# Performance work log

Hardware: AMD Instinct MI355X
Metric: run time of the kernel (lower is better)

Reference implementation:

```python
import jax, jax.numpy as jnp
import numpy as np

# dims
B = 16        # batch
S = 32        # question seq len
H = 768       # bert-base hidden
E = 200000    # num entities
T = 200000    # padded triples per example
R = 500       # num relations
STEPS = 3     # num_steps
WAYS = 2      # num_ways


def setup_inputs() -> dict:
    key = jax.random.key(0)
    ks = jax.random.split(key, 10)
    # one-hot head entity per example (start distribution)
    head_ids = jax.random.randint(ks[0], (B,), 0, E)
    heads = jnp.zeros((B, E), jnp.float32).at[jnp.arange(B), head_ids].set(1.0)
    q_embeddings = jax.random.normal(ks[1], (B, H), jnp.float32)
    q_word_h = jax.random.normal(ks[2], (B, S, H), jnp.float32)
    attention_mask = jnp.ones((B, S), jnp.float32)
    # padded per-example triples (sub, rel, obj)
    sub = jax.random.randint(ks[3], (B, T), 0, E)
    rel = jax.random.randint(ks[4], (B, T), 0, R)
    obj = jax.random.randint(ks[5], (B, T), 0, E)
    triples = jnp.stack([sub, rel, obj], axis=-1).astype(jnp.int32)  # [B,T,3]
    scale = 0.02
    step_W = jax.random.normal(ks[6], (WAYS, STEPS, H, H), jnp.float32) * scale
    step_b = jnp.zeros((WAYS, STEPS, H), jnp.float32)
    rel_W = jax.random.normal(ks[7], (WAYS, H, R), jnp.float32) * scale
    rel_b = jnp.zeros((WAYS, R), jnp.float32)
    hop_W = jax.random.normal(ks[8], (WAYS, H, STEPS), jnp.float32) * scale
    hop_b = jnp.zeros((WAYS, STEPS), jnp.float32)
    return dict(heads=heads, q_embeddings=q_embeddings, q_word_h=q_word_h,
                attention_mask=attention_mask, step_W=step_W, step_b=step_b,
                rel_W=rel_W, rel_b=rel_b, hop_W=hop_W, hop_b=hop_b,
                triples=triples)


def _propagate(last_e, triples, rel_dist):
    # last_e: [E], triples: [T,3], rel_dist: [R] -> [E]
    sub, rel, obj = triples[:, 0], triples[:, 1], triples[:, 2]
    obj_p = last_e[sub] * rel_dist[rel]                 # gather + gate  [T]
    return jax.ops.segment_sum(obj_p, obj, num_segments=E)  # scatter-add [E]


def reference(heads, q_embeddings, q_word_h, attention_mask,
              step_W, step_b, rel_W, rel_b, hop_W, hop_b, triples):
    e_score = []
    for w in range(WAYS):
        last_e = heads                                   # [B,E]
        ent_probs = []
        for t in range(STEPS):
            cq_t = jnp.tanh(q_embeddings @ step_W[w, t] + step_b[w, t])   # [B,H]
            q_logits = jnp.einsum('bh,bsh->bs', cq_t, q_word_h)            # [B,S]
            q_dist = jax.nn.softmax(q_logits, axis=1) * attention_mask
            q_dist = q_dist / (jnp.sum(q_dist, axis=1, keepdims=True) + 1e-6)
            ctx_h = jnp.einsum('bs,bsh->bh', q_dist, q_word_h)             # [B,H]
            rel_dist = jax.nn.sigmoid(ctx_h @ rel_W[w] + rel_b[w])         # [B,R]
            last_e = jax.vmap(_propagate)(last_e, triples, rel_dist)      # [B,E]
            # renormalize entries > 1 (detached divisor, as in original)
            z = jax.lax.stop_gradient(jnp.where(last_e > 1.0, last_e, 1.0))
            last_e = last_e / z
            ent_probs.append(last_e)
        hop_res = jnp.stack(ent_probs, axis=1)                             # [B,STEPS,E]
        hop_attn = jax.nn.softmax(q_embeddings @ hop_W[w] + hop_b[w], axis=1)  # [B,STEPS]
        e_score.append(jnp.einsum('bse,bs->be', hop_res, hop_attn))
    return jnp.prod(jnp.stack(e_score), axis=0)                            # [B,E]
```

## Files before the change

kernel.cpp:

```cpp
#include <hip/hip_runtime.h>
#include <math.h>

#define NB 16
#define NS 32
#define NH 768
#define NE 200000
#define NT 200000
#define NR 500
#define NSTEPS 3
#define NWAYS 2

#define HSZ 2048
#define AHSZ 4096
#define BMW 6272

typedef unsigned int u32;

__device__ __forceinline__ int fhash(int e) { return (int)(((u32)e * 2654435761u) >> 21); }
__device__ __forceinline__ int ahash(int e) { return (int)(((u32)e * 2654435761u) >> 20); }

__global__ __launch_bounds__(256) void dense_kernel(
    const float* __restrict__ qe, const float* __restrict__ qwh,
    const float* __restrict__ mask,
    const float* __restrict__ stepW, const float* __restrict__ stepB,
    const float* __restrict__ relW, const float* __restrict__ relB,
    const float* __restrict__ hopW, const float* __restrict__ hopB,
    float* __restrict__ rel, float* __restrict__ hop)
{
    int blk = blockIdx.x;
    int b = blk % NB;
    int wt = blk / NB;
    int w = wt / NSTEPS;
    int t = wt % NSTEPS;

    __shared__ float s_qe[NH];
    __shared__ float s_part[4][NH];
    __shared__ float s_cq[NH];
    __shared__ float s_ctx[NH];
    __shared__ float s_sm[NS];

    int tid = threadIdx.x;
    int lane = tid & 63, wv = tid >> 6;

    for (int h = tid; h < NH; h += 256) s_qe[h] = qe[b * NH + h];
    __syncthreads();

    {
        const float* W = stepW + (size_t)wt * NH * NH;
        float acc[12];
#pragma unroll
        for (int q = 0; q < 12; ++q) acc[q] = 0.f;
        int h0 = wv * 192;
#pragma unroll 2
        for (int hh = 0; hh < 192; ++hh) {
            int h = h0 + hh;
            float qv = s_qe[h];
            const float* row = W + (size_t)h * NH + lane;
#pragma unroll
            for (int q = 0; q < 12; ++q) acc[q] += qv * row[q * 64];
        }
#pragma unroll
        for (int q = 0; q < 12; ++q) s_part[wv][lane + q * 64] = acc[q];
    }
    __syncthreads();
    for (int j = tid; j < NH; j += 256) {
        float a = s_part[0][j] + s_part[1][j] + s_part[2][j] + s_part[3][j] + stepB[wt * NH + j];
        s_cq[j] = tanhf(a);
    }
    __syncthreads();

    {
        int s = tid >> 3, l = tid & 7;
        const float* row = qwh + ((size_t)b * NS + s) * NH;
        float a = 0.f;
        for (int h = l; h < NH; h += 8) a += s_cq[h] * row[h];
        a += __shfl_down(a, 4, 8);
        a += __shfl_down(a, 2, 8);
        a += __shfl_down(a, 1, 8);
        if (l == 0) s_sm[s] = a;
    }
    __syncthreads();
    if (tid == 0) {
        float mx = -1e30f;
        for (int s = 0; s < NS; ++s) mx = fmaxf(mx, s_sm[s]);
        float sum = 0.f;
        float tmp[NS];
        for (int s = 0; s < NS; ++s) { float ev = expf(s_sm[s] - mx); tmp[s] = ev; sum += ev; }
        float inv = 1.f / sum;
        float sum2 = 0.f;
        for (int s = 0; s < NS; ++s) { float d = tmp[s] * inv * mask[b * NS + s]; tmp[s] = d; sum2 += d; }
        float inv2 = 1.f / (sum2 + 1e-6f);
        for (int s = 0; s < NS; ++s) s_sm[s] = tmp[s] * inv2;
    }
    __syncthreads();

    for (int h = tid; h < NH; h += 256) {
        const float* col = qwh + (size_t)b * NS * NH + h;
        float c = 0.f;
#pragma unroll 8
        for (int s = 0; s < NS; ++s) c += s_sm[s] * col[s * NH];
        s_ctx[h] = c;
    }
    __syncthreads();

    {
        const float* W = relW + (size_t)w * NH * NR;
        float acc[8];
#pragma unroll
        for (int q = 0; q < 8; ++q) acc[q] = 0.f;
        int h0 = wv * 192;
#pragma unroll 2
        for (int hh = 0; hh < 192; ++hh) {
            int h = h0 + hh;
            float cv = s_ctx[h];
            const float* row = W + (size_t)h * NR;
#pragma unroll
            for (int q = 0; q < 8; ++q) {
                int r = lane + q * 64;
                acc[q] += cv * row[r < NR ? r : NR - 1];
            }
        }
#pragma unroll
        for (int q = 0; q < 8; ++q) s_part[wv][lane + q * 64] = acc[q];
    }
    __syncthreads();
    for (int r = tid; r < NR; r += 256) {
        float a = s_part[0][r] + s_part[1][r] + s_part[2][r] + s_part[3][r] + relB[w * NR + r];
        rel[((size_t)wt * NB + b) * NR + r] = 1.f / (1.f + expf(-a));
    }

    if (t == 0) {
        __syncthreads();
        if (wv < 3) {
            float a = 0.f;
            for (int h = lane; h < NH; h += 64) a += s_qe[h] * hopW[((size_t)w * NH + h) * NSTEPS + wv];
            for (int off = 32; off; off >>= 1) a += __shfl_down(a, off, 64);
            if (lane == 0) s_sm[wv] = a + hopB[w * NSTEPS + wv];
        }
        __syncthreads();
        if (tid == 0) {
            float mx = fmaxf(s_sm[0], fmaxf(s_sm[1], s_sm[2]));
            float e0 = expf(s_sm[0] - mx), e1 = expf(s_sm[1] - mx), e2 = expf(s_sm[2] - mx);
            float inv = 1.f / (e0 + e1 + e2);
            hop[(w * NB + b) * NSTEPS + 0] = e0 * inv;
            hop[(w * NB + b) * NSTEPS + 1] = e1 * inv;
            hop[(w * NB + b) * NSTEPS + 2] = e2 * inv;
        }
    }
}

__global__ void head_kernel(const float* __restrict__ heads, int* __restrict__ keys0,
                            float* __restrict__ vals0, u32* __restrict__ bm0)
{
    size_t N4 = (size_t)NB * NE / 4;
    const float4* h4 = (const float4*)heads;
    for (size_t i = (size_t)blockIdx.x * blockDim.x + threadIdx.x; i < N4;
         i += (size_t)gridDim.x * blockDim.x) {
        float4 v = h4[i];
        float c[4] = { v.x, v.y, v.z, v.w };
#pragma unroll
        for (int k = 0; k < 4; ++k) {
            if (c[k] != 0.0f) {
                size_t idx = i * 4 + k;
                int b = (int)(idx / NE);
                int e = (int)(idx % NE);
                int s = fhash(e);
                keys0[(size_t)b * HSZ + s] = e + 1;
                vals0[(size_t)b * HSZ + s] = 1.0f;
                vals0[(size_t)(NB + b) * HSZ + s] = 1.0f;
                atomicOr(&bm0[(size_t)b * BMW + (e >> 5)], 1u << (e & 31));
            }
        }
    }
}

__global__ __launch_bounds__(256) void prop_kernel(
    const int* __restrict__ triples,
    const u32* __restrict__ bmIn, const int* __restrict__ keysIn, const float* __restrict__ valsIn,
    u32* __restrict__ bmOut, int* __restrict__ keysOut, float* __restrict__ valsOut,
    const float* __restrict__ rel, int t)
{
    __shared__ u32 s_bm[BMW];
    int b = blockIdx.x >> 4;
    int c = blockIdx.x & 15;
    const u32* g = bmIn + (size_t)b * BMW;
    for (int k = threadIdx.x; k < BMW; k += 256) s_bm[k] = g[k];
    __syncthreads();

    const int*   kin  = keysIn  + (size_t)b * HSZ;
    const float* v0in = valsIn  + (size_t)b * HSZ;
    const float* v1in = valsIn  + (size_t)(NB + b) * HSZ;
    const float* r0 = rel + ((size_t)(0 * NSTEPS + t) * NB + b) * NR;
    const float* r1 = rel + ((size_t)(1 * NSTEPS + t) * NB + b) * NR;
    int*   kout  = keysOut + (size_t)b * HSZ;
    float* v0out = valsOut + (size_t)b * HSZ;
    float* v1out = valsOut + (size_t)(NB + b) * HSZ;
    u32*   bmo   = bmOut + (size_t)b * BMW;

    const int4* tp = (const int4*)(triples + (size_t)b * NT * 3);
    const int QPC = (NT / 4) / 16;
    int qend = (c + 1) * QPC;
    for (int q = c * QPC + threadIdx.x; q < qend; q += 256) {
        int4 x = tp[q * 3 + 0];
        int4 y = tp[q * 3 + 1];
        int4 z = tp[q * 3 + 2];
        int su[4] = { x.x, x.w, y.z, z.y };
        int re[4] = { x.y, y.x, y.w, z.z };
        int ob[4] = { x.z, y.y, z.x, z.w };
#pragma unroll
        for (int k = 0; k < 4; ++k) {
            int sub = su[k];
            if ((s_bm[sub >> 5] >> (sub & 31)) & 1u) {
                int s = fhash(sub);
                float v0 = 0.f, v1 = 0.f;
                bool found = false;
                for (int p = 0; p < HSZ; ++p) {
                    int kk = kin[s];
                    if (kk == 0) break;
                    if (kk == sub + 1) {
                        v0 = fminf(v0in[s], 1.0f);
                        v1 = fminf(v1in[s], 1.0f);
                        found = true;
                        break;
                    }
                    s = (s + 1) & (HSZ - 1);
                }
                if (found) {
                    float c0 = v0 * r0[re[k]];
                    float c1 = v1 * r1[re[k]];
                    int e = ob[k];
                    int s2 = fhash(e);
                    for (int p = 0; p < HSZ; ++p) {
                        int old = atomicCAS(&kout[s2], 0, e + 1);
                        if (old == 0 || old == e + 1) {
                            atomicAdd(&v0out[s2], c0);
                            atomicAdd(&v1out[s2], c1);
                            if (old == 0) atomicOr(&bmo[e >> 5], 1u << (e & 31));
                            break;
                        }
                        s2 = (s2 + 1) & (HSZ - 1);
                    }
                }
            }
        }
    }
}

__global__ __launch_bounds__(256) void final_kernel(
    const int* __restrict__ keysG, const float* __restrict__ valsG,
    const float* __restrict__ hop, float* __restrict__ out)
{
    __shared__ int s_k[AHSZ];
    __shared__ float s_v0[AHSZ];
    __shared__ float s_v1[AHSZ];
    int b = blockIdx.x;
    for (int i = threadIdx.x; i < AHSZ; i += 256) { s_k[i] = 0; s_v0[i] = 0.f; s_v1[i] = 0.f; }
    __syncthreads();
    for (int gen = 1; gen <= 3; ++gen) {
        const int* kg = keysG + ((size_t)gen * NB + b) * HSZ;
        const float* vg = valsG + (size_t)gen * NWAYS * NB * HSZ;
        const float* v0 = vg + (size_t)b * HSZ;
        const float* v1 = vg + (size_t)(NB + b) * HSZ;
        float h0 = hop[(0 * NB + b) * NSTEPS + (gen - 1)];
        float h1 = hop[(1 * NB + b) * NSTEPS + (gen - 1)];
        for (int i = threadIdx.x; i < HSZ; i += 256) {
            int key = kg[i];
            if (key == 0) continue;
            float a0 = h0 * fminf(v0[i], 1.0f);
            float a1 = h1 * fminf(v1[i], 1.0f);
            int s = ahash(key - 1);
            for (int p = 0; p < AHSZ; ++p) {
                int old = atomicCAS(&s_k[s], 0, key);
                if (old == 0 || old == key) {
                    atomicAdd(&s_v0[s], a0);
                    atomicAdd(&s_v1[s], a1);
                    break;
                }
                s = (s + 1) & (AHSZ - 1);
            }
        }
    }
    __syncthreads();
    for (int i = threadIdx.x; i < AHSZ; i += 256) {
        int key = s_k[i];
        if (key) out[(size_t)b * NE + (key - 1)] = s_v0[i] * s_v1[i];
    }
}

extern "C" void kernel_launch(void* const* d_in, const int* in_sizes, int n_in,
                              void* d_out, int out_size, void* d_ws, size_t ws_size,
                              hipStream_t stream)
{
    const float* heads  = (const float*)d_in[0];
    const float* qe     = (const float*)d_in[1];
    const float* qwh    = (const float*)d_in[2];
    const float* mask   = (const float*)d_in[3];
    const float* stepW  = (const float*)d_in[4];
    const float* stepB  = (const float*)d_in[5];
    const float* relW   = (const float*)d_in[6];
    const float* relB   = (const float*)d_in[7];
    const float* hopW   = (const float*)d_in[8];
    const float* hopB   = (const float*)d_in[9];
    const int*   triples = (const int*)d_in[10];
    float* out = (float*)d_out;

    int*   keysG = (int*)d_ws;
    float* valsG = (float*)(keysG + 4 * NB * HSZ);
    u32*   bmG   = (u32*)(valsG + 4 * NWAYS * NB * HSZ);
    float* rel   = (float*)(bmG + 4 * (size_t)NB * BMW);
    float* hop   = rel + (size_t)NWAYS * NSTEPS * NB * NR;

    size_t zero_bytes = (char*)rel - (char*)d_ws;
    hipMemsetAsync(d_ws, 0, zero_bytes, stream);
    hipMemsetAsync(d_out, 0, (size_t)NB * NE * sizeof(float), stream);

    dense_kernel<<<NWAYS * NSTEPS * NB, 256, 0, stream>>>(
        qe, qwh, mask, stepW, stepB, relW, relB, hopW, hopB, rel, hop);
    head_kernel<<<2048, 256, 0, stream>>>(heads, keysG, valsG, bmG);

    for (int t = 0; t < NSTEPS; ++t) {
        prop_kernel<<<NB * 16, 256, 0, stream>>>(
            triples,
            bmG + (size_t)t * NB * BMW,
            keysG + (size_t)t * NB * HSZ,
            valsG + (size_t)t * NWAYS * NB * HSZ,
            bmG + (size_t)(t + 1) * NB * BMW,
            keysG + (size_t)(t + 1) * NB * HSZ,
            valsG + (size_t)(t + 1) * NWAYS * NB * HSZ,
            rel, t);
    }

    final_kernel<<<NB, 256, 0, stream>>>(keysG, valsG, hop, out);
}
```

Baseline: 255.5 us.

## Split dense kernel into batched GEMM stages and widen propagation grid

The single dense kernel, which re-read each step weight matrix once per batch element, is split into a cq partial GEMM with all 16 batch rows per block, an attention kernel, a batched relation GEMM, and a separate hop kernel. Each weight column is now loaded once and reused across the batch from shared memory, so weight traffic drops by roughly the batch factor. The propagation kernel also uses 25 chunks per example instead of 16, giving more blocks per step. This adds three extra kernel launches and intermediate global buffers for the partial sums and context vectors.

```diff
diff --git a/kernel.cpp b/kernel.cpp
--- a/kernel.cpp
+++ b/kernel.cpp
@@ -13,62 +13,82 @@
 #define HSZ 2048
 #define AHSZ 4096
 #define BMW 6272
+#define PCHUNK 25
 
 typedef unsigned int u32;
 
 __device__ __forceinline__ int fhash(int e) { return (int)(((u32)e * 2654435761u) >> 21); }
 __device__ __forceinline__ int ahash(int e) { return (int)(((u32)e * 2654435761u) >> 20); }
 
-__global__ __launch_bounds__(256) void dense_kernel(
-    const float* __restrict__ qe, const float* __restrict__ qwh,
-    const float* __restrict__ mask,
-    const float* __restrict__ stepW, const float* __restrict__ stepB,
-    const float* __restrict__ relW, const float* __restrict__ relB,
-    const float* __restrict__ hopW, const float* __restrict__ hopB,
-    float* __restrict__ rel, float* __restrict__ hop)
+__global__ __launch_bounds__(256) void cq_part_kernel(
+    const float* __restrict__ qe, const float* __restrict__ stepW,
+    float* __restrict__ part)
 {
     int blk = blockIdx.x;
-    int b = blk % NB;
-    int wt = blk / NB;
-    int w = wt / NSTEPS;
-    int t = wt % NSTEPS;
-
-    __shared__ float s_qe[NH];
-    __shared__ float s_part[4][NH];
+    int jc = blk % 12;
+    int wt = (blk / 12) % 6;
+    int kc = blk / 72;
+
+    __shared__ float s_qe[192 * NB];
+    __shared__ float s_part[2][1024];
+
+    int tid = threadIdx.x;
+    for (int i = tid; i < 192 * NB; i += 256) {
+        int b = i / 192, hh = i % 192;
+        s_qe[hh * NB + b] = qe[b * NH + kc * 192 + hh];
+    }
+    __syncthreads();
+
+    int r = tid & 63, p = tid >> 6;
+    const float* W = stepW + (size_t)wt * NH * NH + (size_t)(kc * 192) * NH + jc * 64 + r;
+    float acc[NB];
+#pragma unroll
+    for (int b = 0; b < NB; ++b) acc[b] = 0.f;
+#pragma unroll 2
+    for (int hh = 0; hh < 48; ++hh) {
+        int h = p * 48 + hh;
+        float w = W[(size_t)h * NH];
+        const float4* q4 = (const float4*)&s_qe[h * NB];
+        float4 qa = q4[0], qb = q4[1], qc = q4[2], qd = q4[3];
+        acc[0]  += w * qa.x; acc[1]  += w * qa.y; acc[2]  += w * qa.z; acc[3]  += w * qa.w;
+        acc[4]  += w * qb.x; acc[5]  += w * qb.y; acc[6]  += w * qb.z; acc[7]  += w * qb.w;
+        acc[8]  += w * qc.x; acc[9]  += w * qc.y; acc[10] += w * qc.z; acc[11] += w * qc.w;
+        acc[12] += w * qd.x; acc[13] += w * qd.y; acc[14] += w * qd.z; acc[15] += w * qd.w;
+    }
+    if (p >= 2) {
+#pragma unroll
+        for (int b = 0; b < NB; ++b) s_part[p - 2][b * 64 + r] = acc[b];
+    }
+    __syncthreads();
+    if (p < 2) {
+#pragma unroll
+        for (int b = 0; b < NB; ++b) s_part[p][b * 64 + r] += acc[b];
+    }
+    __syncthreads();
+    for (int o = tid; o < 1024; o += 256) {
+        int b = o >> 6, rr = o & 63;
+        part[(((size_t)kc * 6 + wt) * NB + b) * NH + jc * 64 + rr] = s_part[0][o] + s_part[1][o];
+    }
+}
+
+__global__ __launch_bounds__(256) void attn_kernel(
+    const float* __restrict__ part, const float* __restrict__ stepB,
+    const float* __restrict__ qwh, const float* __restrict__ mask,
+    float* __restrict__ ctx)
+{
+    int b = blockIdx.x % NB;
+    int wt = blockIdx.x / NB;
     __shared__ float s_cq[NH];
-    __shared__ float s_ctx[NH];
     __shared__ float s_sm[NS];
-
     int tid = threadIdx.x;
-    int lane = tid & 63, wv = tid >> 6;
-
-    for (int h = tid; h < NH; h += 256) s_qe[h] = qe[b * NH + h];
-    __syncthreads();
-
-    {
-        const float* W = stepW + (size_t)wt * NH * NH;
-        float acc[12];
-#pragma unroll
-        for (int q = 0; q < 12; ++q) acc[q] = 0.f;
-        int h0 = wv * 192;
-#pragma unroll 2
-        for (int hh = 0; hh < 192; ++hh) {
-            int h = h0 + hh;
-            float qv = s_qe[h];
-            const float* row = W + (size_t)h * NH + lane;
-#pragma unroll
-            for (int q = 0; q < 12; ++q) acc[q] += qv * row[q * 64];
-        }
-#pragma unroll
-        for (int q = 0; q < 12; ++q) s_part[wv][lane + q * 64] = acc[q];
-    }
-    __syncthreads();
     for (int j = tid; j < NH; j += 256) {
-        float a = s_part[0][j] + s_part[1][j] + s_part[2][j] + s_part[3][j] + stepB[wt * NH + j];
+        float a = stepB[wt * NH + j];
+#pragma unroll
+        for (int kc = 0; kc < 4; ++kc)
+            a += part[(((size_t)kc * 6 + wt) * NB + b) * NH + j];
         s_cq[j] = tanhf(a);
     }
     __syncthreads();
-
     {
         int s = tid >> 3, l = tid & 7;
         const float* row = qwh + ((size_t)b * NS + s) * NH;
@@ -83,8 +103,8 @@
     if (tid == 0) {
         float mx = -1e30f;
         for (int s = 0; s < NS; ++s) mx = fmaxf(mx, s_sm[s]);
+        float tmp[NS];
         float sum = 0.f;
-        float tmp[NS];
         for (int s = 0; s < NS; ++s) { float ev = expf(s_sm[s] - mx); tmp[s] = ev; sum += ev; }
         float inv = 1.f / sum;
         float sum2 = 0.f;
@@ -93,59 +113,88 @@
         for (int s = 0; s < NS; ++s) s_sm[s] = tmp[s] * inv2;
     }
     __syncthreads();
-
     for (int h = tid; h < NH; h += 256) {
         const float* col = qwh + (size_t)b * NS * NH + h;
         float c = 0.f;
 #pragma unroll 8
         for (int s = 0; s < NS; ++s) c += s_sm[s] * col[s * NH];
-        s_ctx[h] = c;
-    }
-    __syncthreads();
-
-    {
-        const float* W = relW + (size_t)w * NH * NR;
-        float acc[8];
-#pragma unroll
-        for (int q = 0; q < 8; ++q) acc[q] = 0.f;
-        int h0 = wv * 192;
+        ctx[((size_t)wt * NB + b) * NH + h] = c;
+    }
+}
+
+__global__ __launch_bounds__(256) void rel_kernel(
+    const float* __restrict__ ctx, const float* __restrict__ relW,
+    const float* __restrict__ relB, float* __restrict__ rel)
+{
+    int wt = blockIdx.x / 8;
+    int rc = blockIdx.x % 8;
+    int w = wt / NSTEPS;
+    __shared__ float s_ctx[NH * NB];
+    __shared__ float s_part[2][1024];
+    int tid = threadIdx.x;
+    for (int i = tid; i < NB * NH; i += 256) {
+        int b = i / NH, h = i % NH;
+        s_ctx[h * NB + b] = ctx[(size_t)wt * NB * NH + i];
+    }
+    __syncthreads();
+    int r = tid & 63, p = tid >> 6;
+    int col = rc * 64 + r;
+    int cl = col < NR ? col : NR - 1;
+    const float* W = relW + (size_t)w * NH * NR + cl;
+    float acc[NB];
+#pragma unroll
+    for (int b = 0; b < NB; ++b) acc[b] = 0.f;
+    int h1 = p * 192 + 192;
 #pragma unroll 2
-        for (int hh = 0; hh < 192; ++hh) {
-            int h = h0 + hh;
-            float cv = s_ctx[h];
-            const float* row = W + (size_t)h * NR;
-#pragma unroll
-            for (int q = 0; q < 8; ++q) {
-                int r = lane + q * 64;
-                acc[q] += cv * row[r < NR ? r : NR - 1];
-            }
+    for (int h = p * 192; h < h1; ++h) {
+        float wv = W[(size_t)h * NR];
+        const float4* q4 = (const float4*)&s_ctx[h * NB];
+        float4 qa = q4[0], qb = q4[1], qc = q4[2], qd = q4[3];
+        acc[0]  += wv * qa.x; acc[1]  += wv * qa.y; acc[2]  += wv * qa.z; acc[3]  += wv * qa.w;
+        acc[4]  += wv * qb.x; acc[5]  += wv * qb.y; acc[6]  += wv * qb.z; acc[7]  += wv * qb.w;
+        acc[8]  += wv * qc.x; acc[9]  += wv * qc.y; acc[10] += wv * qc.z; acc[11] += wv * qc.w;
+        acc[12] += wv * qd.x; acc[13] += wv * qd.y; acc[14] += wv * qd.z; acc[15] += wv * qd.w;
+    }
+    if (p >= 2) {
+#pragma unroll
+        for (int b = 0; b < NB; ++b) s_part[p - 2][b * 64 + r] = acc[b];
+    }
+    __syncthreads();
+    if (p < 2) {
+#pragma unroll
+        for (int b = 0; b < NB; ++b) s_part[p][b * 64 + r] += acc[b];
+    }
+    __syncthreads();
+    for (int o = tid; o < 1024; o += 256) {
+        int b = o >> 6, r2 = o & 63;
+        int cc = rc * 64 + r2;
+        if (cc < NR) {
+            float a = s_part[0][o] + s_part[1][o] + relB[w * NR + cc];
+            rel[((size_t)wt * NB + b) * NR + cc] = 1.f / (1.f + expf(-a));
         }
-#pragma unroll
-        for (int q = 0; q < 8; ++q) s_part[wv][lane + q * 64] = acc[q];
-    }
-    __syncthreads();
-    for (int r = tid; r < NR; r += 256) {
-        float a = s_part[0][r] + s_part[1][r] + s_part[2][r] + s_part[3][r] + relB[w * NR + r];
-        rel[((size_t)wt * NB + b) * NR + r] = 1.f / (1.f + expf(-a));
-    }
-
-    if (t == 0) {
-        __syncthreads();
-        if (wv < 3) {
-            float a = 0.f;
-            for (int h = lane; h < NH; h += 64) a += s_qe[h] * hopW[((size_t)w * NH + h) * NSTEPS + wv];
-            for (int off = 32; off; off >>= 1) a += __shfl_down(a, off, 64);
-            if (lane == 0) s_sm[wv] = a + hopB[w * NSTEPS + wv];
-        }
-        __syncthreads();
-        if (tid == 0) {
-            float mx = fmaxf(s_sm[0], fmaxf(s_sm[1], s_sm[2]));
-            float e0 = expf(s_sm[0] - mx), e1 = expf(s_sm[1] - mx), e2 = expf(s_sm[2] - mx);
-            float inv = 1.f / (e0 + e1 + e2);
-            hop[(w * NB + b) * NSTEPS + 0] = e0 * inv;
-            hop[(w * NB + b) * NSTEPS + 1] = e1 * inv;
-            hop[(w * NB + b) * NSTEPS + 2] = e2 * inv;
-        }
+    }
+}
+
+__global__ __launch_bounds__(192) void hop_kernel(
+    const float* __restrict__ qe, const float* __restrict__ hopW,
+    const float* __restrict__ hopB, float* __restrict__ hop)
+{
+    int wb = blockIdx.x;
+    int w = wb / NB, b = wb % NB;
+    int t = threadIdx.x / 64, l = threadIdx.x % 64;
+    __shared__ float s_logit[4];
+    float a = 0.f;
+    for (int h = l; h < NH; h += 64) a += qe[b * NH + h] * hopW[((size_t)w * NH + h) * NSTEPS + t];
+    for (int off = 32; off; off >>= 1) a += __shfl_down(a, off, 64);
+    if (l == 0) s_logit[t] = a + hopB[w * NSTEPS + t];
+    __syncthreads();
+    if (threadIdx.x == 0) {
+        float mx = fmaxf(s_logit[0], fmaxf(s_logit[1], s_logit[2]));
+        float e0 = expf(s_logit[0] - mx), e1 = expf(s_logit[1] - mx), e2 = expf(s_logit[2] - mx);
+        float inv = 1.f / (e0 + e1 + e2);
+        hop[wb * NSTEPS + 0] = e0 * inv;
+        hop[wb * NSTEPS + 1] = e1 * inv;
+        hop[wb * NSTEPS + 2] = e2 * inv;
     }
 }
 
@@ -181,8 +230,8 @@
     const float* __restrict__ rel, int t)
 {
     __shared__ u32 s_bm[BMW];
-    int b = blockIdx.x >> 4;
-    int c = blockIdx.x & 15;
+    int b = blockIdx.x / PCHUNK;
+    int c = blockIdx.x % PCHUNK;
     const u32* g = bmIn + (size_t)b * BMW;
     for (int k = threadIdx.x; k < BMW; k += 256) s_bm[k] = g[k];
     __syncthreads();
@@ -198,7 +247,7 @@
     u32*   bmo   = bmOut + (size_t)b * BMW;
 
     const int4* tp = (const int4*)(triples + (size_t)b * NT * 3);
-    const int QPC = (NT / 4) / 16;
+    const int QPC = (NT / 4) / PCHUNK;
     int qend = (c + 1) * QPC;
     for (int q = c * QPC + threadIdx.x; q < qend; q += 256) {
         int4 x = tp[q * 3 + 0];
@@ -309,17 +358,21 @@
     u32*   bmG   = (u32*)(valsG + 4 * NWAYS * NB * HSZ);
     float* rel   = (float*)(bmG + 4 * (size_t)NB * BMW);
     float* hop   = rel + (size_t)NWAYS * NSTEPS * NB * NR;
+    float* part  = hop + NWAYS * NB * NSTEPS;
+    float* ctx   = part + (size_t)4 * 6 * NB * NH;
 
     size_t zero_bytes = (char*)rel - (char*)d_ws;
     hipMemsetAsync(d_ws, 0, zero_bytes, stream);
     hipMemsetAsync(d_out, 0, (size_t)NB * NE * sizeof(float), stream);
 
-    dense_kernel<<<NWAYS * NSTEPS * NB, 256, 0, stream>>>(
-        qe, qwh, mask, stepW, stepB, relW, relB, hopW, hopB, rel, hop);
+    cq_part_kernel<<<288, 256, 0, stream>>>(qe, stepW, part);
+    attn_kernel<<<96, 256, 0, stream>>>(part, stepB, qwh, mask, ctx);
+    rel_kernel<<<48, 256, 0, stream>>>(ctx, relW, relB, rel);
+    hop_kernel<<<NWAYS * NB, 192, 0, stream>>>(qe, hopW, hopB, hop);
     head_kernel<<<2048, 256, 0, stream>>>(heads, keysG, valsG, bmG);
 
     for (int t = 0; t < NSTEPS; ++t) {
-        prop_kernel<<<NB * 16, 256, 0, stream>>>(
+        prop_kernel<<<NB * PCHUNK, 256, 0, stream>>>(
             triples,
             bmG + (size_t)t * NB * BMW,
             keysG + (size_t)t * NB * HSZ,
```

After: 256.9 us. Within noise of the previous version (+0.5%).
